# Performance work log

Hardware: AMD Instinct MI355X
Metric: run time of the kernel (lower is better)

Reference implementation:

```python
import jax, jax.numpy as jnp
import numpy as np

D_MODEL = 2048
NUM_HEADS = 16
D_K = D_MODEL // NUM_HEADS
THETA = 10000.0
MAX_SEQ_LEN = 2048
B, S = 2, 2048


def setup_inputs() -> dict:
    key = jax.random.key(0)
    ks = jax.random.split(key, 5)
    x = jax.random.normal(ks[0], (B, S, D_MODEL), dtype=jnp.float32)
    token_positions = jnp.tile(jnp.arange(S, dtype=jnp.int64 if jax.config.jax_enable_x64 else jnp.int32), (B, 1))
    wq = jax.random.normal(ks[1], (D_MODEL, D_MODEL), dtype=jnp.float32)
    wk = jax.random.normal(ks[2], (D_MODEL, D_MODEL), dtype=jnp.float32)
    wv = jax.random.normal(ks[3], (D_MODEL, D_MODEL), dtype=jnp.float32)
    wo = jax.random.normal(ks[4], (D_MODEL, D_MODEL), dtype=jnp.float32)
    return {"x": x, "token_positions": token_positions, "wq": wq, "wk": wk, "wv": wv, "wo": wo}


def _rope_tables():
    # inv freqs: exp(arange(0,d_k,2) * (-log(theta)/d_k))  -> [d_k/2]
    inv_freq = jnp.exp(jnp.arange(0, D_K, 2, dtype=jnp.float32) * (-np.log(THETA) / D_K))
    m = jnp.arange(MAX_SEQ_LEN, dtype=jnp.float32)[:, None]  # [L,1]
    ang = m * inv_freq[None, :]                               # [L, d_k/2]
    return jnp.cos(ang), jnp.sin(ang)


def _apply_rope(x, token_positions, cos_tab, sin_tab):
    # x: [B, H, S, d_k]; token_positions: [B, S]
    cos = cos_tab[token_positions][:, None, :, :]  # [B,1,S,d_k/2]
    sin = sin_tab[token_positions][:, None, :, :]
    xe = x[..., 0::2]
    xo = x[..., 1::2]
    re = xe * cos - xo * sin
    ro = xo * cos + xe * sin
    out = jnp.stack([re, ro], axis=-1).reshape(x.shape)
    return out


def reference(x, token_positions, wq, wk, wv, wo):
    b, s, _ = x.shape
    cos_tab, sin_tab = _rope_tables()

    def split_heads(t):  # [B,S,D] -> [B,H,S,d_k]
        return t.reshape(b, s, NUM_HEADS, D_K).transpose(0, 2, 1, 3)

    q = _apply_rope(split_heads(x @ wq), token_positions, cos_tab, sin_tab)
    k = _apply_rope(split_heads(x @ wk), token_positions, cos_tab, sin_tab)
    v = split_heads(x @ wv)

    scores = jnp.einsum("bhqd,bhkd->bhqk", q, k) / jnp.sqrt(jnp.float32(D_K))
    causal = jnp.tril(jnp.ones((s, s), dtype=bool))
    scores = jnp.where(causal[None, None], scores, jnp.float32(-1e9))
    attn = jax.nn.softmax(scores, axis=-1)
    out = jnp.einsum("bhqk,bhkd->bhqd", attn, v)
    out = out.transpose(0, 2, 1, 3).reshape(b, s, D_MODEL)
    return out @ wo
```

## Files before the change

kernel.cpp:

```cpp
#include <hip/hip_runtime.h>
#include <hip/hip_bf16.h>
#include <cstdio>

namespace {

constexpr int kSeq = 2048;
constexpr int kDModel = 2048;
constexpr int kHeads = 16;
constexpr int kDk = 128;
constexpr int kBatch = 2;
constexpr int kM = kBatch * kSeq;
constexpr float kQScale = 0.08838834764831845f;

typedef __bf16 bf16_t;
typedef __bf16 bf16x8 __attribute__((ext_vector_type(8)));
typedef __bf16 bf16x4 __attribute__((ext_vector_type(4)));
typedef float f32x4 __attribute__((ext_vector_type(4)));
typedef short s16x4 __attribute__((ext_vector_type(4)));

__device__ __forceinline__ f32x4 mfma32(bf16x8 a, bf16x8 b, f32x4 c) {
  return __builtin_amdgcn_mfma_f32_16x16x32_bf16(a, b, c, 0, 0, 0);
}

#if __has_builtin(__builtin_amdgcn_mfma_f32_16x16x16_bf16)
__device__ __forceinline__ f32x4 mfma16(bf16x4 a, bf16x4 b, f32x4 c) {
  return __builtin_amdgcn_mfma_f32_16x16x16_bf16(a, b, c, 0, 0, 0);
}
#else
__device__ __forceinline__ f32x4 mfma16(bf16x4 a, bf16x4 b, f32x4 c) {
  union U { bf16x4 b; s16x4 s; } ua, ub;
  ua.b = a; ub.b = b;
  return __builtin_amdgcn_mfma_f32_16x16x16bf16_1k(ua.s, ub.s, c, 0, 0, 0);
}
#endif

using gas_void = const __attribute__((address_space(1))) void;
using las_void = __attribute__((address_space(3))) void;

__device__ __forceinline__ void gload_lds16(const bf16_t* g, bf16_t* l) {
  __builtin_amdgcn_global_load_lds((gas_void*)g, (las_void*)l, 16, 0, 0);
}

__global__ void k_rope_table(float* __restrict__ cost, float* __restrict__ sint) {
  const int p = blockIdx.x;
  const int i = threadIdx.x;
  const double inv = exp(-(double)(2 * i) * 9.210340371976184 / 128.0);
  const double ang = (double)p * inv;
  cost[p * 64 + i] = (float)cos(ang);
  sint[p * 64 + i] = (float)sin(ang);
}

__global__ void k_split_x(const float* __restrict__ x, bf16_t* __restrict__ xh,
                          bf16_t* __restrict__ xl, int n) {
  const int idx = (blockIdx.x * blockDim.x + threadIdx.x) * 4;
  if (idx >= n) return;
  const float4 v = *(const float4*)(x + idx);
  const float vv[4] = {v.x, v.y, v.z, v.w};
  bf16x4 hv, lv;
#pragma unroll
  for (int j = 0; j < 4; ++j) {
    const bf16_t h = (bf16_t)vv[j];
    hv[j] = h;
    lv[j] = (bf16_t)(vv[j] - (float)h);
  }
  *(bf16x4*)(xh + idx) = hv;
  *(bf16x4*)(xl + idx) = lv;
}

__global__ void k_transpose_w(const float* __restrict__ w, bf16_t* __restrict__ wth,
                              bf16_t* __restrict__ wtl) {
  __shared__ float tile[32][33];
  const int bx = blockIdx.x * 32;
  const int by = blockIdx.y * 32;
  const int tx = threadIdx.x, ty = threadIdx.y;
#pragma unroll
  for (int i = 0; i < 32; i += 8)
    tile[ty + i][tx] = w[(size_t)(by + ty + i) * kDModel + bx + tx];
  __syncthreads();
#pragma unroll
  for (int i = 0; i < 32; i += 8) {
    const float v = tile[tx][ty + i];
    const size_t o = (size_t)(bx + ty + i) * kDModel + by + tx;
    const bf16_t h = (bf16_t)v;
    wth[o] = h;
    if (wtl) wtl[o] = (bf16_t)(v - (float)h);
  }
}

__global__ __launch_bounds__(512, 2) void k_gemmqk(
    const bf16_t* __restrict__ Ah, const bf16_t* __restrict__ Al,
    const bf16_t* __restrict__ Bh, const bf16_t* __restrict__ Bl,
    bf16_t* __restrict__ Qh, bf16_t* __restrict__ Ql,
    bf16_t* __restrict__ Kh, bf16_t* __restrict__ Kl,
    const int* __restrict__ tokpos, const float* __restrict__ cost,
    const float* __restrict__ sint) {
  __shared__ __align__(16) bf16_t sA[3][512 * 32];
  __shared__ __align__(16) bf16_t sB[3][128 * 32];
  constexpr int ntk = 192;

  const int tid = threadIdx.x;
  const int wid = tid >> 6, lane = tid & 63;
  const int lo = lane & 15, hi = lane >> 4;
  const int wr = wid >> 1, wc = wid & 1;

  const int bid = blockIdx.x;
  const int wgid = (bid & 7) * 32 + (bid >> 3);
  const int mt = wgid >> 5, nt = wgid & 31;
  const int m0 = mt * 512, n0 = nt * 128;

  const int sr = tid >> 2;
  const int sc = ((tid & 3) ^ (sr & 3)) * 8;
  size_t offA[4];
#pragma unroll
  for (int ui = 0; ui < 4; ++ui)
    offA[ui] = (size_t)(m0 + ui * 128 + sr) * 2048 + sc;
  const size_t offB = (size_t)(n0 + sr) * 2048 + sc;
  const int ldsT = wid * 512;

  auto STAGE = [&](int slot, int tt) {
    const bf16_t *As, *Bs;
    int kb;
    if (tt < 64) {
      As = Ah; Bs = Bh; kb = tt * 32;
    } else if (tt < 128) {
      As = Ah; Bs = Bl; kb = (tt - 64) * 32;
    } else {
      As = Al; Bs = Bh; kb = (tt - 128) * 32;
    }
    bf16_t* dA = sA[slot] + ldsT;
#pragma unroll
    for (int ui = 0; ui < 4; ++ui)
      gload_lds16(As + offA[ui] + kb, dA + ui * 4096);
    gload_lds16(Bs + offB + kb, sB[slot] + ldsT);
  };

  int aoff[8], boff[4];
#pragma unroll
  for (int mi = 0; mi < 8; ++mi)
    aoff[mi] = (wr * 128 + mi * 16 + lo) * 32 + ((hi ^ (lo & 3)) * 8);
#pragma unroll
  for (int ni = 0; ni < 4; ++ni)
    boff[ni] = (wc * 64 + ni * 16 + lo) * 32 + ((hi ^ (lo & 3)) * 8);

  f32x4 acc[8][4];
  const f32x4 z = {0.f, 0.f, 0.f, 0.f};
#pragma unroll
  for (int i = 0; i < 8; ++i)
#pragma unroll
    for (int j = 0; j < 4; ++j) acc[i][j] = z;

  STAGE(0, 0);
  STAGE(1, 1);
  asm volatile("s_waitcnt vmcnt(5)" ::: "memory");
  __builtin_amdgcn_s_barrier();
  __builtin_amdgcn_sched_barrier(0);

  int s0 = 0;
#pragma unroll 1
  for (int t = 0; t < ntk; ++t) {
    const bf16_t* sa = sA[s0];
    const bf16_t* sb = sB[s0];
    int s2 = s0 + 2;
    if (s2 >= 3) s2 -= 3;

    bf16x8 af[8], bfr[4];
#pragma unroll
    for (int mi = 0; mi < 4; ++mi) af[mi] = *(const bf16x8*)(sa + aoff[mi]);
#pragma unroll
    for (int ni = 0; ni < 4; ++ni) bfr[ni] = *(const bf16x8*)(sb + boff[ni]);
    if (t + 2 < ntk) STAGE(s2, t + 2);
#pragma unroll
    for (int mi = 4; mi < 8; ++mi) af[mi] = *(const bf16x8*)(sa + aoff[mi]);

    if (t + 3 < ntk)
      asm volatile("s_waitcnt vmcnt(5)" ::: "memory");
    else
      asm volatile("s_waitcnt vmcnt(0)" ::: "memory");
    asm volatile("s_waitcnt lgkmcnt(0)" ::: "memory");
    __builtin_amdgcn_s_barrier();
    __builtin_amdgcn_sched_barrier(0);

    __builtin_amdgcn_s_setprio(1);
#pragma unroll
    for (int ni = 0; ni < 4; ++ni)
#pragma unroll
      for (int mi = 0; mi < 8; ++mi)
        acc[mi][ni] = mfma32(af[mi], bfr[ni], acc[mi][ni]);
    __builtin_amdgcn_s_setprio(0);

    s0 += 1;
    if (s0 >= 3) s0 = 0;
  }

  const int qk = n0 >> 11;
  bf16_t* Xh = qk ? Kh : Qh;
  bf16_t* Xl = qk ? Kl : Ql;
  const float scale = qk ? 1.0f : kQScale;
  const int is64 = (tokpos[1] == 0) ? 1 : 0;
#pragma unroll
  for (int mi = 0; mi < 8; ++mi) {
#pragma unroll
    for (int r = 0; r < 4; ++r) {
      const int row = m0 + wr * 128 + mi * 16 + hi * 4 + r;
      const int pos = is64 ? tokpos[2 * row] : tokpos[row];
#pragma unroll
      for (int ni = 0; ni < 4; ++ni) {
        const int col = n0 + wc * 64 + ni * 16 + lo;
        const float v = acc[mi][ni][r] * scale;
        const float pv = __shfl_xor(v, 1);
        const int ip = (col & 127) >> 1;
        const float c = cost[pos * 64 + ip];
        const float sn = sint[pos * 64 + ip];
        const float sgn = (lo & 1) ? sn : -sn;
        const float rv = v * c + pv * sgn;
        const bf16_t hb = (bf16_t)rv;
        const size_t o = (size_t)row * 2048 + (col & 2047);
        Xh[o] = hb;
        Xl[o] = (bf16_t)(rv - (float)hb);
      }
    }
  }
}

template <int EPI>
__global__ __launch_bounds__(512) void k_gemm8(
    const bf16_t* __restrict__ Ah, const bf16_t* __restrict__ Bh,
    void* __restrict__ O0, int NT, int ntk) {
  __shared__ __align__(16) bf16_t sA[3][256 * 64];
  __shared__ __align__(16) bf16_t sB[3][128 * 64];

  const int tid = threadIdx.x;
  const int wid = tid >> 6, lane = tid & 63;
  const int lo = lane & 15, hi = lane >> 4;
  const int wrr = wid >> 1, wcc = wid & 1;
  const int x7 = lo & 7;

  const int bid = blockIdx.x;
  const int wgid = (bid & 7) * (gridDim.x >> 3) + (bid >> 3);
  const int mt = wgid / NT, nt = wgid % NT;
  const int m0 = mt * 256, n0 = nt * 128;

  const int rB = tid >> 3;
  const int ch8 = ((tid & 7) ^ (rB & 7)) * 8;
  size_t offA[4], offB[2];
#pragma unroll
  for (int u = 0; u < 2; ++u)
#pragma unroll
    for (int i = 0; i < 2; ++i)
      offA[u * 2 + i] = (size_t)(m0 + u * 128 + i * 64 + rB) * 2048 + ch8;
#pragma unroll
  for (int i = 0; i < 2; ++i)
    offB[i] = (size_t)(n0 + i * 64 + rB) * 2048 + ch8;
  const int ldsOff = wid * 512;

  auto STAGE_A = [&](int slot, int t) {
    const bf16_t* base = Ah + t * 64;
    bf16_t* d = sA[slot] + ldsOff;
#pragma unroll
    for (int ui = 0; ui < 4; ++ui) gload_lds16(base + offA[ui], d + ui * 4096);
  };
  auto STAGE_B = [&](int slot, int t) {
    const bf16_t* base = Bh + t * 64;
    bf16_t* d = sB[slot] + ldsOff;
#pragma unroll
    for (int i = 0; i < 2; ++i) gload_lds16(base + offB[i], d + i * 4096);
  };

  int aoff[4][2], boff[4][2];
#pragma unroll
  for (int mi = 0; mi < 4; ++mi)
#pragma unroll
    for (int ks = 0; ks < 2; ++ks)
      aoff[mi][ks] = (wrr * 64 + mi * 16 + lo) * 64 + (((ks * 4 + hi) ^ x7) * 8);
#pragma unroll
  for (int ni = 0; ni < 4; ++ni)
#pragma unroll
    for (int ks = 0; ks < 2; ++ks)
      boff[ni][ks] = (wcc * 64 + ni * 16 + lo) * 64 + (((ks * 4 + hi) ^ x7) * 8);

  f32x4 acc[4][4];
  const f32x4 z = {0.f, 0.f, 0.f, 0.f};
#pragma unroll
  for (int i = 0; i < 4; ++i)
#pragma unroll
    for (int j = 0; j < 4; ++j) acc[i][j] = z;

  STAGE_A(0, 0);
  STAGE_B(0, 0);
  STAGE_A(1, 1);
  STAGE_B(1, 1);
  asm volatile("s_waitcnt vmcnt(6)" ::: "memory");
  __builtin_amdgcn_s_barrier();
  asm volatile("" ::: "memory");

  int s0 = 0;
  for (int t = 0; t < ntk; ++t) {
    const bf16_t* sa = sA[s0];
    const bf16_t* sb = sB[s0];
    int s2 = s0 + 2;
    if (s2 >= 3) s2 -= 3;
    const bool pf = (t + 2 < ntk);

    bf16x8 af[2][2], bfr[4][2];
#pragma unroll
    for (int mi = 0; mi < 2; ++mi)
#pragma unroll
      for (int ks = 0; ks < 2; ++ks)
        af[mi][ks] = *(const bf16x8*)(sa + aoff[mi][ks]);
#pragma unroll
    for (int ni = 0; ni < 4; ++ni)
#pragma unroll
      for (int ks = 0; ks < 2; ++ks)
        bfr[ni][ks] = *(const bf16x8*)(sb + boff[ni][ks]);
    if (pf) STAGE_A(s2, t + 2);
    asm volatile("" ::: "memory");
    __builtin_amdgcn_s_barrier();
    asm volatile("" ::: "memory");
    __builtin_amdgcn_s_setprio(1);
#pragma unroll
    for (int ni = 0; ni < 4; ++ni)
#pragma unroll
      for (int mi = 0; mi < 2; ++mi)
#pragma unroll
        for (int ks = 0; ks < 2; ++ks)
          acc[mi][ni] = mfma32(af[mi][ks], bfr[ni][ks], acc[mi][ni]);
    __builtin_amdgcn_s_setprio(0);

    bf16x8 ag[2][2];
#pragma unroll
    for (int mi = 0; mi < 2; ++mi)
#pragma unroll
      for (int ks = 0; ks < 2; ++ks)
        ag[mi][ks] = *(const bf16x8*)(sa + aoff[2 + mi][ks]);
    if (pf) STAGE_B(s2, t + 2);
    if (pf)
      asm volatile("s_waitcnt vmcnt(6)" ::: "memory");
    else
      asm volatile("s_waitcnt vmcnt(0)" ::: "memory");
    __builtin_amdgcn_s_barrier();
    asm volatile("" ::: "memory");
    __builtin_amdgcn_s_setprio(1);
#pragma unroll
    for (int ni = 0; ni < 4; ++ni)
#pragma unroll
      for (int mi = 0; mi < 2; ++mi)
#pragma unroll
        for (int ks = 0; ks < 2; ++ks)
          acc[2 + mi][ni] = mfma32(ag[mi][ks], bfr[ni][ks], acc[2 + mi][ni]);
    __builtin_amdgcn_s_setprio(0);

    s0 += 1;
    if (s0 >= 3) s0 = 0;
  }

  if constexpr (EPI == 0) {
    float* C = (float*)O0;
#pragma unroll
    for (int mi = 0; mi < 4; ++mi)
#pragma unroll
      for (int ni = 0; ni < 4; ++ni)
#pragma unroll
        for (int r = 0; r < 4; ++r) {
          const int row = m0 + wrr * 64 + mi * 16 + hi * 4 + r;
          const int col = n0 + wcc * 64 + ni * 16 + lo;
          C[(size_t)row * 2048 + col] = acc[mi][ni][r];
        }
  } else {
    bf16_t* VT = (bf16_t*)O0;
#pragma unroll
    for (int mi = 0; mi < 4; ++mi)
#pragma unroll
      for (int ni = 0; ni < 4; ++ni) {
        const int col = n0 + wcc * 64 + ni * 16 + lo;
        const int h = col >> 7, d = col & 127;
        const int rowb = m0 + wrr * 64 + mi * 16 + hi * 4;
        const int b = rowb >> 11, s = rowb & (kSeq - 1);
        bf16x4 ov;
#pragma unroll
        for (int r = 0; r < 4; ++r) ov[r] = (bf16_t)acc[mi][ni][r];
        *(bf16x4*)(VT + ((size_t)((b * kHeads + h) * kDk + d)) * kSeq + s) = ov;
      }
  }
}

__global__ __launch_bounds__(512, 2) void k_attn4(
    const bf16_t* __restrict__ Qh, const bf16_t* __restrict__ Ql,
    const bf16_t* __restrict__ Kh, const bf16_t* __restrict__ Kl,
    const bf16_t* __restrict__ VT, bf16_t* __restrict__ Ob) {
  __shared__ __align__(16) bf16_t sK[2][2][64 * 128];
  __shared__ __align__(16) bf16_t sV[2][128 * 64];

  const int tid = threadIdx.x;
  const int wid = tid >> 6, lane = tid & 63;
  const int lo = lane & 15, hi = lane >> 4;
  const int flat = blockIdx.x;
  const int j = flat >> 3;
  const int bh = (flat & 7) * 4 + (j & 3);
  const int p = j >> 2;
  const int b = bh >> 4, h = bh & 15;
  const int qiW = (wid < 4) ? (15 - p) : p;
  const int qw = qiW * 128 + (wid & 3) * 32;
  const int nkv = 2 * (15 - p) + 2;

  bf16x8 qhf[4][2], qlf[4][2];
  {
    const size_t qbase =
        (size_t)(b * kSeq + qw + lo) * kDModel + h * kDk + hi * 8;
#pragma unroll
    for (int qt = 0; qt < 2; ++qt)
#pragma unroll
      for (int ks = 0; ks < 4; ++ks) {
        const size_t o = qbase + (size_t)qt * 16 * kDModel + ks * 32;
        qhf[ks][qt] = *(const bf16x8*)(Qh + o);
        qlf[ks][qt] = *(const bf16x8*)(Ql + o);
      }
  }

  const int rK0 = wid * 8 + (lane >> 4);
  const int gK0 = ((lane & 15) ^ (rK0 & 15)) * 8;
  const int gK1 = ((lane & 15) ^ ((rK0 + 4) & 15)) * 8;
  const bf16_t* pKh0 = Kh + (size_t)(b * kSeq + rK0) * kDModel + h * kDk + gK0;
  const bf16_t* pKh1 = Kh + (size_t)(b * kSeq + rK0 + 4) * kDModel + h * kDk + gK1;
  const bf16_t* pKl0 = Kl + (pKh0 - Kh);
  const bf16_t* pKl1 = Kl + (pKh1 - Kh);
  const int dV0 = wid * 16 + (lane >> 3);
  const int gV0 = ((lane & 7) ^ (dV0 & 7)) * 8;
  const int gV1 = ((lane & 7) ^ ((dV0 + 8) & 7)) * 8;
  const bf16_t* pV0 = VT + (size_t)(bh * kDk + dV0) * kSeq + gV0;
  const bf16_t* pV1 = VT + (size_t)(bh * kDk + dV0 + 8) * kSeq + gV1;
  const int ldsK = (wid * 8) * 128;
  const int ldsV = (wid * 16) * 64;

  f32x4 of[8][2];
  const f32x4 z = {0.f, 0.f, 0.f, 0.f};
#pragma unroll
  for (int di = 0; di < 8; ++di) {
    of[di][0] = z;
    of[di][1] = z;
  }
  float m[2] = {-3e38f, -3e38f};
  float l[2] = {0.f, 0.f};

  auto STAGE = [&](int buf, int t) {
    const size_t ko = (size_t)t * 64 * kDModel;
    const size_t vo = (size_t)t * 64;
    bf16_t* dk = sK[buf][0] + ldsK;
    bf16_t* dl = sK[buf][1] + ldsK;
    gload_lds16(pKh0 + ko, dk);
    gload_lds16(pKh1 + ko, dk + 512);
    gload_lds16(pKl0 + ko, dl);
    gload_lds16(pKl1 + ko, dl + 512);
    bf16_t* dv = sV[buf] + ldsV;
    gload_lds16(pV0 + vo, dv);
    gload_lds16(pV1 + vo, dv + 512);
  };

  STAGE(0, 0);
  __syncthreads();

  for (int t = 0; t < nkv; ++t) {
    const int kv0 = t * 64;
    if (t + 1 < nkv) STAGE((t + 1) & 1, t + 1);

    if (kv0 <= qw + 31) {
      const bf16_t* bKh = sK[t & 1][0];
      const bf16_t* bKl = sK[t & 1][1];
      const bf16_t* bV = sV[t & 1];
      const bool maskedw = (kv0 + 63 > qw);

      f32x4 st[4][2];
#pragma unroll
      for (int kt = 0; kt < 4; ++kt) {
        st[kt][0] = z;
        st[kt][1] = z;
      }
#pragma unroll
      for (int kt = 0; kt < 4; ++kt) {
#pragma unroll
        for (int ks = 0; ks < 4; ++ks) {
          const int krow = kt * 16 + lo;
          const int ka = krow * 128 + (((ks * 4 + hi) ^ (krow & 15)) * 8);
          const bf16x8 kh8 = *(const bf16x8*)(bKh + ka);
          const bf16x8 kl8 = *(const bf16x8*)(bKl + ka);
#pragma unroll
          for (int qt = 0; qt < 2; ++qt) {
            st[kt][qt] = mfma32(kh8, qhf[ks][qt], st[kt][qt]);
            st[kt][qt] = mfma32(kh8, qlf[ks][qt], st[kt][qt]);
            st[kt][qt] = mfma32(kl8, qhf[ks][qt], st[kt][qt]);
          }
        }
      }

      bf16x4 pb[4][2];
#pragma unroll
      for (int qt = 0; qt < 2; ++qt) {
        const int q = qw + qt * 16 + lo;
        float mt = -3e38f;
#pragma unroll
        for (int kt = 0; kt < 4; ++kt)
#pragma unroll
          for (int r = 0; r < 4; ++r) {
            float s = st[kt][qt][r];
            if (maskedw && (kv0 + kt * 16 + hi * 4 + r > q)) s = -1e30f;
            st[kt][qt][r] = s;
            mt = fmaxf(mt, s);
          }
        mt = fmaxf(mt, __shfl_xor(mt, 16));
        mt = fmaxf(mt, __shfl_xor(mt, 32));
        if (!__all(mt <= m[qt] + 8.f)) {
          const float mnew = fmaxf(m[qt], mt);
          const float corr = __expf(m[qt] - mnew);
          l[qt] *= corr;
#pragma unroll
          for (int di = 0; di < 8; ++di) of[di][qt] = of[di][qt] * corr;
          m[qt] = mnew;
        }
        float rs = 0.f;
#pragma unroll
        for (int kt = 0; kt < 4; ++kt) {
          bf16x4 pv;
#pragma unroll
          for (int r = 0; r < 4; ++r) {
            const float pp = __expf(st[kt][qt][r] - m[qt]);
            rs += pp;
            pv[r] = (bf16_t)pp;
          }
          pb[kt][qt] = pv;
        }
        rs += __shfl_xor(rs, 16);
        rs += __shfl_xor(rs, 32);
        l[qt] += rs;
      }

#pragma unroll
      for (int di = 0; di < 8; ++di) {
        const int d = di * 16 + lo;
#pragma unroll
        for (int kt = 0; kt < 4; ++kt) {
          const int va =
              d * 64 + (((kt * 2 + (hi >> 1)) ^ (d & 7)) * 8) + (hi & 1) * 4;
          const bf16x4 vf = *(const bf16x4*)(bV + va);
          of[di][0] = mfma16(vf, pb[kt][0], of[di][0]);
          of[di][1] = mfma16(vf, pb[kt][1], of[di][1]);
        }
      }
    }
    __syncthreads();
  }

#pragma unroll
  for (int qt = 0; qt < 2; ++qt) {
    const float linv = 1.f / l[qt];
    const size_t ob =
        (size_t)(b * kSeq + qw + qt * 16 + lo) * kDModel + h * kDk + hi * 4;
#pragma unroll
    for (int di = 0; di < 8; ++di) {
      bf16x4 ov;
#pragma unroll
      for (int r = 0; r < 4; ++r) ov[r] = (bf16_t)(of[di][qt][r] * linv);
      *(bf16x4*)(Ob + ob + di * 16) = ov;
    }
  }
}

}

extern "C" void kernel_launch(void* const* d_in, const int* in_sizes, int n_in,
                              void* d_out, int out_size, void* d_ws, size_t ws_size,
                              hipStream_t stream) {
  (void)in_sizes; (void)n_in; (void)out_size;
  const float* x = (const float*)d_in[0];
  const int* tokpos = (const int*)d_in[1];
  const float* wq = (const float*)d_in[2];
  const float* wk = (const float*)d_in[3];
  const float* wv = (const float*)d_in[4];
  const float* wo = (const float*)d_in[5];
  float* out = (float*)d_out;

  char* p = (char*)d_ws;
  auto take = [&](size_t bytes) { char* q = p; p += bytes; return q; };
  float* cost = (float*)take((size_t)kSeq * 64 * sizeof(float));
  float* sint = (float*)take((size_t)kSeq * 64 * sizeof(float));
  const size_t mat = (size_t)kM * kDModel * sizeof(bf16_t);
  const size_t wmat = (size_t)kDModel * kDModel * sizeof(bf16_t);
  bf16_t* xh = (bf16_t*)take(mat);
  bf16_t* xl = (bf16_t*)take(mat);
  bf16_t* wqkth = (bf16_t*)take(2 * wmat);
  bf16_t* wqktl = (bf16_t*)take(2 * wmat);
  bf16_t* wvt = (bf16_t*)take(wmat);
  bf16_t* wot = (bf16_t*)take(wmat);
  bf16_t* qh = (bf16_t*)take(mat);
  bf16_t* ql = (bf16_t*)take(mat);
  bf16_t* kh = (bf16_t*)take(mat);
  bf16_t* kl = (bf16_t*)take(mat);
  bf16_t* vt = (bf16_t*)take(mat);
  bf16_t* ob = (bf16_t*)take(mat);
  if ((size_t)(p - (char*)d_ws) > ws_size) {
    fprintf(stderr, "MHA: workspace too small: need %zu have %zu\n",
            (size_t)(p - (char*)d_ws), ws_size);
    return;
  }

  k_rope_table<<<dim3(kSeq), dim3(64), 0, stream>>>(cost, sint);
  k_split_x<<<dim3((kM * kDModel) / (256 * 4)), dim3(256), 0, stream>>>(
      x, xh, xl, kM * kDModel);
  {
    dim3 tb(32, 8), tg(kDModel / 32, kDModel / 32);
    k_transpose_w<<<tg, tb, 0, stream>>>(wq, wqkth, wqktl);
    k_transpose_w<<<tg, tb, 0, stream>>>(wk, wqkth + (size_t)2048 * 2048,
                                         wqktl + (size_t)2048 * 2048);
    k_transpose_w<<<tg, tb, 0, stream>>>(wv, wvt, nullptr);
    k_transpose_w<<<tg, tb, 0, stream>>>(wo, wot, nullptr);
  }
  k_gemmqk<<<dim3(256), dim3(512), 0, stream>>>(xh, xl, wqkth, wqktl, qh, ql,
                                                kh, kl, tokpos, cost, sint);
  k_gemm8<2><<<dim3(256), dim3(512), 0, stream>>>(xh, wvt, vt, 16, 32);
  k_attn4<<<dim3(256), dim3(512), 0, stream>>>(qh, ql, kh, kl, vt, ob);
  k_gemm8<0><<<dim3(256), dim3(512), 0, stream>>>(ob, wot, out, 16, 32);
}
```

Before: 479.3 us.

## Retile QK projection GEMM to square 256x256 tiles with BK=64 double buffering

The fused Q/K projection GEMM moves from 512x128 block tiles with BK=32 triple buffering to 256x256 tiles with BK=64 and double buffering. Waves are arranged 2x4, and each iteration runs two k-substeps of MFMAs with an 8-way XOR swizzle on the LDS layout. The square tile gives more even A/B reuse per block and halves the number of barrier iterations. In exchange, prefetch depth drops from two stages to one, so global-load latency has less room to hide behind compute, and LDS use per block rises.

```diff
diff --git a/kernel.cpp b/kernel.cpp
--- a/kernel.cpp
+++ b/kernel.cpp
@@ -87,60 +87,67 @@
   }
 }
 
-__global__ __launch_bounds__(512, 2) void k_gemmqk(
+__global__ __launch_bounds__(512, 2) void k_gemmw(
     const bf16_t* __restrict__ Ah, const bf16_t* __restrict__ Al,
     const bf16_t* __restrict__ Bh, const bf16_t* __restrict__ Bl,
     bf16_t* __restrict__ Qh, bf16_t* __restrict__ Ql,
     bf16_t* __restrict__ Kh, bf16_t* __restrict__ Kl,
     const int* __restrict__ tokpos, const float* __restrict__ cost,
     const float* __restrict__ sint) {
-  __shared__ __align__(16) bf16_t sA[3][512 * 32];
-  __shared__ __align__(16) bf16_t sB[3][128 * 32];
-  constexpr int ntk = 192;
+  __shared__ __align__(16) bf16_t sA[2][256 * 64];
+  __shared__ __align__(16) bf16_t sB[2][256 * 64];
+  constexpr int ntk = 96;
 
   const int tid = threadIdx.x;
   const int wid = tid >> 6, lane = tid & 63;
   const int lo = lane & 15, hi = lane >> 4;
-  const int wr = wid >> 1, wc = wid & 1;
+  const int wr = wid >> 2, wc = wid & 3;
 
   const int bid = blockIdx.x;
   const int wgid = (bid & 7) * 32 + (bid >> 3);
-  const int mt = wgid >> 5, nt = wgid & 31;
-  const int m0 = mt * 512, n0 = nt * 128;
-
-  const int sr = tid >> 2;
-  const int sc = ((tid & 3) ^ (sr & 3)) * 8;
-  size_t offA[4];
-#pragma unroll
-  for (int ui = 0; ui < 4; ++ui)
-    offA[ui] = (size_t)(m0 + ui * 128 + sr) * 2048 + sc;
-  const size_t offB = (size_t)(n0 + sr) * 2048 + sc;
-  const int ldsT = wid * 512;
+  const int m0 = (wgid >> 4) * 256, n0 = (wgid & 15) * 256;
+
+  const int srow = tid >> 3;
+  const int gch = ((tid & 7) ^ (srow & 7)) * 8;
+  size_t offA[4], offB[4];
+#pragma unroll
+  for (int i = 0; i < 4; ++i) {
+    offA[i] = (size_t)(m0 + i * 64 + srow) * 2048 + gch;
+    offB[i] = (size_t)(n0 + i * 64 + srow) * 2048 + gch;
+  }
 
   auto STAGE = [&](int slot, int tt) {
-    const bf16_t *As, *Bs;
-    int kb;
-    if (tt < 64) {
-      As = Ah; Bs = Bh; kb = tt * 32;
-    } else if (tt < 128) {
-      As = Ah; Bs = Bl; kb = (tt - 64) * 32;
+    const bf16_t* As;
+    const bf16_t* Bs;
+    if (tt < 32) {
+      As = Ah; Bs = Bh;
+    } else if (tt < 64) {
+      As = Ah; Bs = Bl;
     } else {
-      As = Al; Bs = Bh; kb = (tt - 128) * 32;
+      As = Al; Bs = Bh;
     }
-    bf16_t* dA = sA[slot] + ldsT;
-#pragma unroll
-    for (int ui = 0; ui < 4; ++ui)
-      gload_lds16(As + offA[ui] + kb, dA + ui * 4096);
-    gload_lds16(Bs + offB + kb, sB[slot] + ldsT);
+    const int kb = (tt & 31) * 64;
+#pragma unroll
+    for (int i = 0; i < 4; ++i)
+      gload_lds16(As + offA[i] + kb, sA[slot] + i * 4096 + wid * 512);
+#pragma unroll
+    for (int i = 0; i < 4; ++i)
+      gload_lds16(Bs + offB[i] + kb, sB[slot] + i * 4096 + wid * 512);
   };
 
-  int aoff[8], boff[4];
+  int aoff[8][2], boff[4][2];
 #pragma unroll
   for (int mi = 0; mi < 8; ++mi)
-    aoff[mi] = (wr * 128 + mi * 16 + lo) * 32 + ((hi ^ (lo & 3)) * 8);
+#pragma unroll
+    for (int ks = 0; ks < 2; ++ks)
+      aoff[mi][ks] =
+          (wr * 128 + mi * 16 + lo) * 64 + (((ks * 4 + hi) ^ (lo & 7)) * 8);
 #pragma unroll
   for (int ni = 0; ni < 4; ++ni)
-    boff[ni] = (wc * 64 + ni * 16 + lo) * 32 + ((hi ^ (lo & 3)) * 8);
+#pragma unroll
+    for (int ks = 0; ks < 2; ++ks)
+      boff[ni][ks] =
+          (wc * 64 + ni * 16 + lo) * 64 + (((ks * 4 + hi) ^ (lo & 7)) * 8);
 
   f32x4 acc[8][4];
   const f32x4 z = {0.f, 0.f, 0.f, 0.f};
@@ -150,46 +157,49 @@
     for (int j = 0; j < 4; ++j) acc[i][j] = z;
 
   STAGE(0, 0);
-  STAGE(1, 1);
-  asm volatile("s_waitcnt vmcnt(5)" ::: "memory");
+  asm volatile("s_waitcnt vmcnt(0)" ::: "memory");
   __builtin_amdgcn_s_barrier();
   __builtin_amdgcn_sched_barrier(0);
 
-  int s0 = 0;
 #pragma unroll 1
   for (int t = 0; t < ntk; ++t) {
-    const bf16_t* sa = sA[s0];
-    const bf16_t* sb = sB[s0];
-    int s2 = s0 + 2;
-    if (s2 >= 3) s2 -= 3;
-
-    bf16x8 af[8], bfr[4];
-#pragma unroll
-    for (int mi = 0; mi < 4; ++mi) af[mi] = *(const bf16x8*)(sa + aoff[mi]);
-#pragma unroll
-    for (int ni = 0; ni < 4; ++ni) bfr[ni] = *(const bf16x8*)(sb + boff[ni]);
-    if (t + 2 < ntk) STAGE(s2, t + 2);
-#pragma unroll
-    for (int mi = 4; mi < 8; ++mi) af[mi] = *(const bf16x8*)(sa + aoff[mi]);
-
-    if (t + 3 < ntk)
-      asm volatile("s_waitcnt vmcnt(5)" ::: "memory");
-    else
-      asm volatile("s_waitcnt vmcnt(0)" ::: "memory");
+    const bf16_t* sa = sA[t & 1];
+    const bf16_t* sb = sB[t & 1];
+
+    bf16x8 a0[8], b0[4];
+#pragma unroll
+    for (int mi = 0; mi < 8; ++mi) a0[mi] = *(const bf16x8*)(sa + aoff[mi][0]);
+#pragma unroll
+    for (int ni = 0; ni < 4; ++ni) b0[ni] = *(const bf16x8*)(sb + boff[ni][0]);
+    if (t + 1 < ntk) STAGE((t + 1) & 1, t + 1);
     asm volatile("s_waitcnt lgkmcnt(0)" ::: "memory");
+    __builtin_amdgcn_sched_barrier(0);
+    __builtin_amdgcn_s_setprio(1);
+#pragma unroll
+    for (int ni = 0; ni < 4; ++ni)
+#pragma unroll
+      for (int mi = 0; mi < 8; ++mi)
+        acc[mi][ni] = mfma32(a0[mi], b0[ni], acc[mi][ni]);
+    __builtin_amdgcn_s_setprio(0);
+
+    bf16x8 a1[8], b1[4];
+#pragma unroll
+    for (int mi = 0; mi < 8; ++mi) a1[mi] = *(const bf16x8*)(sa + aoff[mi][1]);
+#pragma unroll
+    for (int ni = 0; ni < 4; ++ni) b1[ni] = *(const bf16x8*)(sb + boff[ni][1]);
+    asm volatile("s_waitcnt lgkmcnt(0)" ::: "memory");
+    __builtin_amdgcn_sched_barrier(0);
+    __builtin_amdgcn_s_setprio(1);
+#pragma unroll
+    for (int ni = 0; ni < 4; ++ni)
+#pragma unroll
+      for (int mi = 0; mi < 8; ++mi)
+        acc[mi][ni] = mfma32(a1[mi], b1[ni], acc[mi][ni]);
+    __builtin_amdgcn_s_setprio(0);
+
+    asm volatile("s_waitcnt vmcnt(0)" ::: "memory");
     __builtin_amdgcn_s_barrier();
     __builtin_amdgcn_sched_barrier(0);
-
-    __builtin_amdgcn_s_setprio(1);
-#pragma unroll
-    for (int ni = 0; ni < 4; ++ni)
-#pragma unroll
-      for (int mi = 0; mi < 8; ++mi)
-        acc[mi][ni] = mfma32(af[mi], bfr[ni], acc[mi][ni]);
-    __builtin_amdgcn_s_setprio(0);
-
-    s0 += 1;
-    if (s0 >= 3) s0 = 0;
   }
 
   const int qk = n0 >> 11;
@@ -612,8 +622,8 @@
     k_transpose_w<<<tg, tb, 0, stream>>>(wv, wvt, nullptr);
     k_transpose_w<<<tg, tb, 0, stream>>>(wo, wot, nullptr);
   }
-  k_gemmqk<<<dim3(256), dim3(512), 0, stream>>>(xh, xl, wqkth, wqktl, qh, ql,
-                                                kh, kl, tokpos, cost, sint);
+  k_gemmw<<<dim3(256), dim3(512), 0, stream>>>(xh, xl, wqkth, wqktl, qh, ql,
+                                               kh, kl, tokpos, cost, sint);
   k_gemm8<2><<<dim3(256), dim3(512), 0, stream>>>(xh, wvt, vt, 16, 32);
   k_attn4<<<dim3(256), dim3(512), 0, stream>>>(qh, ql, kh, kl, vt, ob);
   k_gemm8<0><<<dim3(256), dim3(512), 0, stream>>>(ob, wot, out, 16, 32);
```

New measurement: 539.6 us. 12.6% more time.

## Shrink QK GEMM tile to 256x128 with 256 threads and double buffering

Applied to the files above, without the earlier changes.

Replaces the 512x128-tile, 512-thread, triple-buffered QK projection GEMM with a 256x128-tile, 256-thread kernel launched on 512 blocks. It uses two LDS buffers with plain __syncthreads instead of hand-tuned waitcnt, barrier and priority control, and adjusts the LDS swizzle to match the new row layout. The aim is more blocks, smaller LDS use and higher occupancy, at the cost of less A/B reuse per block and less latency hiding from the simpler pipeline.

```diff
diff --git a/kernel.cpp b/kernel.cpp
--- a/kernel.cpp
+++ b/kernel.cpp
@@ -87,15 +87,15 @@
   }
 }
 
-__global__ __launch_bounds__(512, 2) void k_gemmqk(
+__global__ __launch_bounds__(256, 2) void k_gemmqk2(
     const bf16_t* __restrict__ Ah, const bf16_t* __restrict__ Al,
     const bf16_t* __restrict__ Bh, const bf16_t* __restrict__ Bl,
     bf16_t* __restrict__ Qh, bf16_t* __restrict__ Ql,
     bf16_t* __restrict__ Kh, bf16_t* __restrict__ Kl,
     const int* __restrict__ tokpos, const float* __restrict__ cost,
     const float* __restrict__ sint) {
-  __shared__ __align__(16) bf16_t sA[3][512 * 32];
-  __shared__ __align__(16) bf16_t sB[3][128 * 32];
+  __shared__ __align__(16) bf16_t sA[2][256 * 32];
+  __shared__ __align__(16) bf16_t sB[2][128 * 32];
   constexpr int ntk = 192;
 
   const int tid = threadIdx.x;
@@ -104,43 +104,47 @@
   const int wr = wid >> 1, wc = wid & 1;
 
   const int bid = blockIdx.x;
-  const int wgid = (bid & 7) * 32 + (bid >> 3);
+  const int wgid = (bid & 7) * 64 + (bid >> 3);
   const int mt = wgid >> 5, nt = wgid & 31;
-  const int m0 = mt * 512, n0 = nt * 128;
+  const int m0 = mt * 256, n0 = nt * 128;
 
   const int sr = tid >> 2;
-  const int sc = ((tid & 3) ^ (sr & 3)) * 8;
+  const int sc = ((tid & 3) ^ ((sr >> 1) & 3)) * 8;
   size_t offA[4];
 #pragma unroll
   for (int ui = 0; ui < 4; ++ui)
-    offA[ui] = (size_t)(m0 + ui * 128 + sr) * 2048 + sc;
-  const size_t offB = (size_t)(n0 + sr) * 2048 + sc;
-  const int ldsT = wid * 512;
+    offA[ui] = (size_t)(m0 + ui * 64 + sr) * 2048 + sc;
+  size_t offB[2];
+#pragma unroll
+  for (int i = 0; i < 2; ++i)
+    offB[i] = (size_t)(n0 + i * 64 + sr) * 2048 + sc;
 
   auto STAGE = [&](int slot, int tt) {
     const bf16_t *As, *Bs;
-    int kb;
     if (tt < 64) {
-      As = Ah; Bs = Bh; kb = tt * 32;
+      As = Ah; Bs = Bh;
     } else if (tt < 128) {
-      As = Ah; Bs = Bl; kb = (tt - 64) * 32;
+      As = Ah; Bs = Bl;
     } else {
-      As = Al; Bs = Bh; kb = (tt - 128) * 32;
+      As = Al; Bs = Bh;
     }
-    bf16_t* dA = sA[slot] + ldsT;
+    const int kb = (tt & 63) * 32;
 #pragma unroll
     for (int ui = 0; ui < 4; ++ui)
-      gload_lds16(As + offA[ui] + kb, dA + ui * 4096);
-    gload_lds16(Bs + offB + kb, sB[slot] + ldsT);
+      gload_lds16(As + offA[ui] + kb, sA[slot] + ui * 2048 + tid * 8);
+#pragma unroll
+    for (int i = 0; i < 2; ++i)
+      gload_lds16(Bs + offB[i] + kb, sB[slot] + i * 2048 + tid * 8);
   };
 
+  const int xq = (lo >> 1) & 3;
   int aoff[8], boff[4];
 #pragma unroll
   for (int mi = 0; mi < 8; ++mi)
-    aoff[mi] = (wr * 128 + mi * 16 + lo) * 32 + ((hi ^ (lo & 3)) * 8);
+    aoff[mi] = (wr * 128 + mi * 16 + lo) * 32 + ((hi ^ xq) * 8);
 #pragma unroll
   for (int ni = 0; ni < 4; ++ni)
-    boff[ni] = (wc * 64 + ni * 16 + lo) * 32 + ((hi ^ (lo & 3)) * 8);
+    boff[ni] = (wc * 64 + ni * 16 + lo) * 32 + ((hi ^ xq) * 8);
 
   f32x4 acc[8][4];
   const f32x4 z = {0.f, 0.f, 0.f, 0.f};
@@ -150,46 +154,24 @@
     for (int j = 0; j < 4; ++j) acc[i][j] = z;
 
   STAGE(0, 0);
-  STAGE(1, 1);
-  asm volatile("s_waitcnt vmcnt(5)" ::: "memory");
-  __builtin_amdgcn_s_barrier();
-  __builtin_amdgcn_sched_barrier(0);
-
-  int s0 = 0;
+  __syncthreads();
+
 #pragma unroll 1
   for (int t = 0; t < ntk; ++t) {
-    const bf16_t* sa = sA[s0];
-    const bf16_t* sb = sB[s0];
-    int s2 = s0 + 2;
-    if (s2 >= 3) s2 -= 3;
-
+    if (t + 1 < ntk) STAGE((t + 1) & 1, t + 1);
+    const bf16_t* sa = sA[t & 1];
+    const bf16_t* sb = sB[t & 1];
     bf16x8 af[8], bfr[4];
 #pragma unroll
-    for (int mi = 0; mi < 4; ++mi) af[mi] = *(const bf16x8*)(sa + aoff[mi]);
+    for (int mi = 0; mi < 8; ++mi) af[mi] = *(const bf16x8*)(sa + aoff[mi]);
 #pragma unroll
     for (int ni = 0; ni < 4; ++ni) bfr[ni] = *(const bf16x8*)(sb + boff[ni]);
-    if (t + 2 < ntk) STAGE(s2, t + 2);
-#pragma unroll
-    for (int mi = 4; mi < 8; ++mi) af[mi] = *(const bf16x8*)(sa + aoff[mi]);
-
-    if (t + 3 < ntk)
-      asm volatile("s_waitcnt vmcnt(5)" ::: "memory");
-    else
-      asm volatile("s_waitcnt vmcnt(0)" ::: "memory");
-    asm volatile("s_waitcnt lgkmcnt(0)" ::: "memory");
-    __builtin_amdgcn_s_barrier();
-    __builtin_amdgcn_sched_barrier(0);
-
-    __builtin_amdgcn_s_setprio(1);
 #pragma unroll
     for (int ni = 0; ni < 4; ++ni)
 #pragma unroll
       for (int mi = 0; mi < 8; ++mi)
         acc[mi][ni] = mfma32(af[mi], bfr[ni], acc[mi][ni]);
-    __builtin_amdgcn_s_setprio(0);
-
-    s0 += 1;
-    if (s0 >= 3) s0 = 0;
+    __syncthreads();
   }
 
   const int qk = n0 >> 11;
@@ -612,8 +594,8 @@
     k_transpose_w<<<tg, tb, 0, stream>>>(wv, wvt, nullptr);
     k_transpose_w<<<tg, tb, 0, stream>>>(wo, wot, nullptr);
   }
-  k_gemmqk<<<dim3(256), dim3(512), 0, stream>>>(xh, xl, wqkth, wqktl, qh, ql,
-                                                kh, kl, tokpos, cost, sint);
+  k_gemmqk2<<<dim3(512), dim3(256), 0, stream>>>(xh, xl, wqkth, wqktl, qh, ql,
+                                                 kh, kl, tokpos, cost, sint);
   k_gemm8<2><<<dim3(256), dim3(512), 0, stream>>>(xh, wvt, vt, 16, 32);
   k_attn4<<<dim3(256), dim3(512), 0, stream>>>(qh, ql, kh, kl, vt, ob);
   k_gemm8<0><<<dim3(256), dim3(512), 0, stream>>>(ob, wot, out, 16, 32);
```

Result: slower. 620.2 us (+29.4%).
